# Kernel optimization log

Measured on AMD Instinct MI355X. Metric: run time of the kernel, lower is better.

The kernel has to match this reference:

```python
import jax, jax.numpy as jnp
import numpy as np

HEADS = 12
HEAD_SIZE = 64
NEG = 1e12


def setup_inputs() -> dict:
    key = jax.random.key(0)
    k1, k2 = jax.random.split(key)
    B, L, D = 32, 512, 768
    x = jax.random.normal(k1, (B, L, D), dtype=jnp.float32)
    mask = jnp.ones((B, L), dtype=jnp.float32)  # padding mask (1 = valid)
    W = jax.random.normal(k2, (D, HEADS * HEAD_SIZE * 2), dtype=jnp.float32) * 0.02
    b = jnp.zeros((HEADS * HEAD_SIZE * 2,), dtype=jnp.float32)
    return {"x": x, "mask": mask, "W": W, "b": b}


def _rope_sin_cos(L, s, dtype):
    # bert4keras SinusoidalPositionEmbedding: pe[..., ::2] = sin, pe[..., 1::2] = cos
    pos = jnp.arange(L, dtype=dtype)
    freq = jnp.power(10000.0, -2.0 * jnp.arange(s // 2, dtype=dtype) / s)
    ang = pos[:, None] * freq[None, :]            # [L, s/2]
    sin = jnp.repeat(jnp.sin(ang), 2, axis=-1)    # [L, s]
    cos = jnp.repeat(jnp.cos(ang), 2, axis=-1)    # [L, s]
    return sin, cos


def _rotate_half(t):
    # interleaved rotation: (-t1, t0, -t3, t2, ...)
    t2 = jnp.stack([-t[..., 1::2], t[..., ::2]], axis=-1)
    return t2.reshape(t.shape)


def reference(x, mask, W, b):
    B, L, D = x.shape
    s = HEAD_SIZE
    proj = x @ W + b                               # [B, L, heads*2s]
    proj = proj.reshape(B, L, HEADS, 2 * s)        # split-into-heads + stack
    qw, kw = proj[..., :s], proj[..., s:]
    sin, cos = _rope_sin_cos(L, s, x.dtype)
    sin = sin[None, :, None, :]                    # [1, L, 1, s]
    cos = cos[None, :, None, :]
    qw = qw * cos + _rotate_half(qw) * sin
    kw = kw * cos + _rotate_half(kw) * sin
    logits = jnp.einsum('bmhs,bnhs->bhmn', qw, kw)  # [B, H, L, L]
    m2 = mask[:, None, :, None]
    m3 = mask[:, None, None, :]
    logits = logits * m2 + (1.0 - m2) * -NEG
    logits = logits * m3 + (1.0 - m3) * -NEG
    tril = jnp.tril(jnp.ones((L, L), dtype=logits.dtype), -1)  # strictly lower
    logits = logits - tril * NEG                    # keep upper-triangular spans
    return (logits / jnp.sqrt(jnp.asarray(s, logits.dtype))).reshape(B, HEADS, L * L)
```

## Files before the change

kernel.cpp:

```cpp
#include <hip/hip_runtime.h>
#include <hip/hip_bf16.h>

#define HEADS 12
#define HSIZE 64
#define BATCH 32
#define SEQ 512
#define DIM 768
#define NOUT 1536
#define MROWS 16384
#define NEGV 1e12f

typedef __bf16 bf16x8 __attribute__((ext_vector_type(8)));
typedef float f32x4 __attribute__((ext_vector_type(4)));
typedef unsigned short u16x8 __attribute__((ext_vector_type(8)));
typedef unsigned short u16x4 __attribute__((ext_vector_type(4)));

__device__ __forceinline__ void async16(const void* g, void* l) {
  __builtin_amdgcn_global_load_lds(
      (const __attribute__((address_space(1))) void*)g,
      (__attribute__((address_space(3))) void*)l, 16, 0, 0);
}

__device__ __forceinline__ unsigned short f2b(float f) {
  union { __hip_bfloat16 h; unsigned short u; } cv;
  cv.h = __float2bfloat16(f);
  return cv.u;
}

__global__ void rope_table(float* __restrict__ sin_t, float* __restrict__ cos_t) {
  int idx = blockIdx.x * 256 + threadIdx.x;
  if (idx < SEQ * 32) {
    int pos = idx >> 5;
    int i = idx & 31;
    float freq = powf(10000.0f, -2.0f * (float)i / 64.0f);
    float ang = (float)pos * freq;
    sin_t[idx] = sinf(ang);
    cos_t[idx] = cosf(ang);
  }
}

__global__ void convert_x(const float* __restrict__ x, unsigned short* __restrict__ xb) {
  int idx = blockIdx.x * 256 + threadIdx.x;
  float4 v = ((const float4*)x)[idx];
  ushort4 o;
  o.x = f2b(v.x); o.y = f2b(v.y); o.z = f2b(v.z); o.w = f2b(v.w);
  ((ushort4*)xb)[idx] = o;
}

__global__ void transpose_w(const float* __restrict__ W, unsigned short* __restrict__ Wt) {
  __shared__ unsigned short tile[32][33];
  int n0 = blockIdx.x * 32;
  int k0 = blockIdx.y * 32;
  int tx = threadIdx.x & 31, ty = threadIdx.x >> 5;
#pragma unroll
  for (int j = 0; j < 32; j += 8) {
    tile[ty + j][tx] = f2b(W[(size_t)(k0 + ty + j) * NOUT + n0 + tx]);
  }
  __syncthreads();
#pragma unroll
  for (int j = 0; j < 32; j += 8) {
    Wt[(size_t)(n0 + ty + j) * DIM + k0 + tx] = tile[tx][ty + j];
  }
}

__global__ __launch_bounds__(256) void gemm_rope(
    const unsigned short* __restrict__ xb, const unsigned short* __restrict__ wt,
    const float* __restrict__ bias, const float* __restrict__ sin_t,
    const float* __restrict__ cos_t, unsigned short* __restrict__ q_ws,
    unsigned short* __restrict__ k_ws) {
  __shared__ __align__(16) unsigned short smem[128 * 136];
  unsigned short* As = smem;
  unsigned short* Bs = smem + 8192;
  const int tid = threadIdx.x;
  const int bx = blockIdx.x;
  const int tn = (bx % (NOUT / 128)) * 128;
  const int tm = (bx / (NOUT / 128)) * 128;
  const int wid = tid >> 6, lane = tid & 63;
  const int wm = (wid >> 1) * 64, wn = (wid & 1) * 64;
  const int lrow = lane & 15, lk = (lane >> 4) * 8;

  const int sr = tid >> 3;
  const int scb = (tid & 7) * 8;
  const unsigned short* a_src = xb + (size_t)(tm + sr) * DIM + scb;
  const unsigned short* b_src = wt + (size_t)(tn + sr) * DIM + scb;

  f32x4 acc[4][4] = {};
  for (int kt = 0; kt < 12; ++kt) {
    const int k0 = kt * 64;
#pragma unroll
    for (int p = 0; p < 4; ++p) {
      async16(a_src + (size_t)(p * 32) * DIM + k0, &As[(p * 32 + sr) * 64 + scb]);
      async16(b_src + (size_t)(p * 32) * DIM + k0, &Bs[(p * 32 + sr) * 64 + scb]);
    }
    __syncthreads();
#pragma unroll
    for (int ks = 0; ks < 2; ++ks) {
      bf16x8 nf[4], mf[4];
#pragma unroll
      for (int i = 0; i < 4; ++i) {
        nf[i] = *(const bf16x8*)&Bs[(wn + i * 16 + lrow) * 64 + ks * 32 + lk];
        mf[i] = *(const bf16x8*)&As[(wm + i * 16 + lrow) * 64 + ks * 32 + lk];
      }
#pragma unroll
      for (int ai = 0; ai < 4; ++ai)
#pragma unroll
        for (int bi = 0; bi < 4; ++bi)
          acc[ai][bi] = __builtin_amdgcn_mfma_f32_16x16x32_bf16(
              nf[ai], mf[bi], acc[ai][bi], 0, 0, 0);
    }
    __syncthreads();
  }

#pragma unroll
  for (int ai = 0; ai < 4; ++ai) {
    const int nloc = wn + ai * 16 + (lane >> 4) * 4;
    const int colb = tn + nloc;
    const int d0 = colb & 63;
    const float4 b4 = *(const float4*)&bias[colb];
#pragma unroll
    for (int bi = 0; bi < 4; ++bi) {
      const int mloc = wm + bi * 16 + lrow;
      const int pos = (tm + mloc) & (SEQ - 1);
      const float2 s01 = *(const float2*)&sin_t[pos * 32 + (d0 >> 1)];
      const float2 c01 = *(const float2*)&cos_t[pos * 32 + (d0 >> 1)];
      const float v0 = acc[ai][bi][0] + b4.x;
      const float v1 = acc[ai][bi][1] + b4.y;
      const float v2 = acc[ai][bi][2] + b4.z;
      const float v3 = acc[ai][bi][3] + b4.w;
      u16x4 pk;
      pk[0] = f2b(fmaf(v0, c01.x, -v1 * s01.x));
      pk[1] = f2b(fmaf(v1, c01.x,  v0 * s01.x));
      pk[2] = f2b(fmaf(v2, c01.y, -v3 * s01.y));
      pk[3] = f2b(fmaf(v3, c01.y,  v2 * s01.y));
      *(u16x4*)&smem[mloc * 136 + nloc] = pk;
    }
  }
  __syncthreads();

  const int bq = tm >> 9;
  const int pos0 = tm & (SEQ - 1);
  const int head = tn >> 7;
  const size_t rowbase = ((size_t)(bq * HEADS + head) * SEQ + pos0);
  const int rr = tid >> 3;
  const int cc = tid & 7;
#pragma unroll
  for (int p = 0; p < 4; ++p) {
    const int r = p * 32 + rr;
    u16x8 vq = *(const u16x8*)&smem[r * 136 + cc * 8];
    u16x8 vk = *(const u16x8*)&smem[r * 136 + 64 + cc * 8];
    *(u16x8*)&q_ws[(rowbase + r) * 64 + cc * 8] = vq;
    *(u16x8*)&k_ws[(rowbase + r) * 64 + cc * 8] = vk;
  }
}

__global__ __launch_bounds__(256) void qk_kernel(
    const unsigned short* __restrict__ q_ws, const unsigned short* __restrict__ k_ws,
    const float* __restrict__ mask, float* __restrict__ out) {
  __shared__ __align__(16) float ot[128 * 68];
  const int bx = blockIdx.x;
  const int bh = bx >> 2;
  const int tmm = (bx & 3) * 128;
  const int bidx = bh / HEADS;
  const int tid = threadIdx.x, wid = tid >> 6, lane = tid & 63;
  const int wm = wid * 32;
  const int lrow = lane & 15, lk = (lane >> 4) * 8;
  const unsigned short* Q = q_ws + ((size_t)bh << 15);
  const unsigned short* K = k_ws + ((size_t)bh << 15);

  bf16x8 qf[2][2];
#pragma unroll
  for (int mi = 0; mi < 2; ++mi)
#pragma unroll
    for (int ks = 0; ks < 2; ++ks)
      qf[mi][ks] = *(const bf16x8*)&Q[(size_t)(tmm + wm + mi * 16 + lrow) * 64 + ks * 32 + lk];

  float* obase = out + ((size_t)bh << 18);
  const float* mrow = mask + (size_t)bidx * SEQ;
  const int cc = tid & 15;
  const int rr = tid >> 4;

  for (int t = 0; t < 4; ++t) {
    const int tnn = t * 128;
    bf16x8 kf[8][2];
#pragma unroll
    for (int ni = 0; ni < 8; ++ni)
#pragma unroll
      for (int ks = 0; ks < 2; ++ks)
        kf[ni][ks] = *(const bf16x8*)&K[(size_t)(tnn + ni * 16 + lrow) * 64 + ks * 32 + lk];

    f32x4 acc[8][2] = {};
#pragma unroll
    for (int ks = 0; ks < 2; ++ks)
#pragma unroll
      for (int ni = 0; ni < 8; ++ni)
#pragma unroll
        for (int mi = 0; mi < 2; ++mi)
          acc[ni][mi] = __builtin_amdgcn_mfma_f32_16x16x32_bf16(
              kf[ni][ks], qf[mi][ks], acc[ni][mi], 0, 0, 0);

#pragma unroll
    for (int h = 0; h < 2; ++h) {
      __syncthreads();
#pragma unroll
      for (int ai = 0; ai < 4; ++ai) {
        const int nloc = ai * 16 + (lane >> 4) * 4;
#pragma unroll
        for (int mi = 0; mi < 2; ++mi) {
          const int mloc = wm + mi * 16 + lrow;
          *(f32x4*)&ot[mloc * 68 + nloc] = acc[h * 4 + ai][mi];
        }
      }
      __syncthreads();
      const int n0 = tnn + h * 64 + cc * 4;
      const f32x4 m3v = *(const f32x4*)&mrow[n0];
#pragma unroll
      for (int p = 0; p < 8; ++p) {
        const int r = p * 16 + rr;
        const int m = tmm + r;
        f32x4 v = *(const f32x4*)&ot[r * 68 + cc * 4];
        const float m2 = mrow[m];
        f32x4 o;
#pragma unroll
        for (int j = 0; j < 4; ++j) {
          float vv = v[j];
          vv = vv * m2 + (1.0f - m2) * (-NEGV);
          vv = vv * m3v[j] + (1.0f - m3v[j]) * (-NEGV);
          if (m > n0 + j) vv -= NEGV;
          o[j] = vv * 0.125f;
        }
        __builtin_nontemporal_store(o, (f32x4*)&obase[(size_t)m * 512 + n0]);
      }
    }
  }
}

extern "C" void kernel_launch(void* const* d_in, const int* in_sizes, int n_in,
                              void* d_out, int out_size, void* d_ws, size_t ws_size,
                              hipStream_t stream) {
  const float* x = (const float*)d_in[0];
  const float* mask = (const float*)d_in[1];
  const float* W = (const float*)d_in[2];
  const float* b = (const float*)d_in[3];
  float* out = (float*)d_out;

  char* ws = (char*)d_ws;
  float* sin_t = (float*)(ws + 0);
  float* cos_t = (float*)(ws + 65536);
  unsigned short* xb  = (unsigned short*)(ws + 131072);
  unsigned short* wt  = (unsigned short*)(ws + 25296896);
  unsigned short* q_ws = (unsigned short*)(ws + 27656192);
  unsigned short* k_ws = (unsigned short*)(ws + 52822016);

  rope_table<<<dim3(64), dim3(256), 0, stream>>>(sin_t, cos_t);
  convert_x<<<dim3(MROWS * DIM / 4 / 256), dim3(256), 0, stream>>>(x, xb);
  transpose_w<<<dim3(NOUT / 32, DIM / 32), dim3(256), 0, stream>>>(W, wt);
  gemm_rope<<<dim3((MROWS / 128) * (NOUT / 128)), dim3(256), 0, stream>>>(
      xb, wt, b, sin_t, cos_t, q_ws, k_ws);
  qk_kernel<<<dim3(BATCH * HEADS * 4), dim3(256), 0, stream>>>(q_ws, k_ws, mask, out);
}
```

Before: 519.3 us.

## Switch projection GEMM to FP8 MFMA with swizzled LDS layout

Converts x and W to FP8 (e4m3) instead of bf16 and runs the projection GEMM with the scaled 16x16x128 f8f6f4 MFMA, halving the K-loop trip count and the operand bytes loaded into LDS. It adds an XOR swizzle on LDS slots to avoid bank conflicts. FP8 sharply reduces input precision, so logits could drift beyond tolerance. The output qk kernel, which dominates the write traffic, is unchanged.

```diff
diff --git a/kernel.cpp b/kernel.cpp
--- a/kernel.cpp
+++ b/kernel.cpp
@@ -12,6 +12,8 @@
 
 typedef __bf16 bf16x8 __attribute__((ext_vector_type(8)));
 typedef float f32x4 __attribute__((ext_vector_type(4)));
+typedef int i32x4 __attribute__((ext_vector_type(4)));
+typedef int i32x8 __attribute__((ext_vector_type(8)));
 typedef unsigned short u16x8 __attribute__((ext_vector_type(8)));
 typedef unsigned short u16x4 __attribute__((ext_vector_type(4)));
 
@@ -25,6 +27,13 @@
   union { __hip_bfloat16 h; unsigned short u; } cv;
   cv.h = __float2bfloat16(f);
   return cv.u;
+}
+
+__device__ __forceinline__ unsigned int pk4_fp8(float a, float b, float c, float d) {
+  int v = 0;
+  v = __builtin_amdgcn_cvt_pk_fp8_f32(a, b, v, false);
+  v = __builtin_amdgcn_cvt_pk_fp8_f32(c, d, v, true);
+  return (unsigned int)v;
 }
 
 __global__ void rope_table(float* __restrict__ sin_t, float* __restrict__ cos_t) {
@@ -39,78 +48,98 @@
   }
 }
 
-__global__ void convert_x(const float* __restrict__ x, unsigned short* __restrict__ xb) {
+__global__ void convert_x(const float* __restrict__ x, unsigned int* __restrict__ xf8) {
   int idx = blockIdx.x * 256 + threadIdx.x;
-  float4 v = ((const float4*)x)[idx];
-  ushort4 o;
-  o.x = f2b(v.x); o.y = f2b(v.y); o.z = f2b(v.z); o.w = f2b(v.w);
-  ((ushort4*)xb)[idx] = o;
-}
-
-__global__ void transpose_w(const float* __restrict__ W, unsigned short* __restrict__ Wt) {
-  __shared__ unsigned short tile[32][33];
+  float4 v0 = ((const float4*)x)[idx * 2];
+  float4 v1 = ((const float4*)x)[idx * 2 + 1];
+  uint2 o;
+  o.x = pk4_fp8(v0.x, v0.y, v0.z, v0.w);
+  o.y = pk4_fp8(v1.x, v1.y, v1.z, v1.w);
+  ((uint2*)xf8)[idx] = o;
+}
+
+__global__ void transpose_w(const float* __restrict__ W, unsigned char* __restrict__ Wt) {
+  __shared__ float tile[32][33];
   int n0 = blockIdx.x * 32;
   int k0 = blockIdx.y * 32;
   int tx = threadIdx.x & 31, ty = threadIdx.x >> 5;
 #pragma unroll
   for (int j = 0; j < 32; j += 8) {
-    tile[ty + j][tx] = f2b(W[(size_t)(k0 + ty + j) * NOUT + n0 + tx]);
+    tile[ty + j][tx] = W[(size_t)(k0 + ty + j) * NOUT + n0 + tx];
   }
   __syncthreads();
 #pragma unroll
   for (int j = 0; j < 32; j += 8) {
-    Wt[(size_t)(n0 + ty + j) * DIM + k0 + tx] = tile[tx][ty + j];
+    const int n = n0 + ty + j;
+    Wt[(size_t)n * DIM + k0 + tx] =
+        (unsigned char)(pk4_fp8(tile[tx][ty + j], 0.f, 0.f, 0.f) & 0xFF);
   }
 }
 
 __global__ __launch_bounds__(256) void gemm_rope(
-    const unsigned short* __restrict__ xb, const unsigned short* __restrict__ wt,
+    const unsigned char* __restrict__ xf8, const unsigned char* __restrict__ wf8,
     const float* __restrict__ bias, const float* __restrict__ sin_t,
     const float* __restrict__ cos_t, unsigned short* __restrict__ q_ws,
     unsigned short* __restrict__ k_ws) {
-  __shared__ __align__(16) unsigned short smem[128 * 136];
-  unsigned short* As = smem;
-  unsigned short* Bs = smem + 8192;
+  __shared__ __align__(16) unsigned char smem[128 * 136 * 2];
+  unsigned char* As = smem;
+  unsigned char* Bs = smem + 16384;
   const int tid = threadIdx.x;
   const int bx = blockIdx.x;
   const int tn = (bx % (NOUT / 128)) * 128;
   const int tm = (bx / (NOUT / 128)) * 128;
   const int wid = tid >> 6, lane = tid & 63;
   const int wm = (wid >> 1) * 64, wn = (wid & 1) * 64;
-  const int lrow = lane & 15, lk = (lane >> 4) * 8;
-
-  const int sr = tid >> 3;
-  const int scb = (tid & 7) * 8;
-  const unsigned short* a_src = xb + (size_t)(tm + sr) * DIM + scb;
-  const unsigned short* b_src = wt + (size_t)(tn + sr) * DIM + scb;
+  const int lrow = lane & 15;
+  const int kc = lane >> 4;
+
+  const int srow = tid >> 3;
+  const int sslot = (tid & 7) ^ (srow & 7);
+  const unsigned char* a_src = xf8 + (size_t)(tm + srow) * DIM + sslot * 16;
+  const unsigned char* b_src = wf8 + (size_t)(tn + srow) * DIM + sslot * 16;
+  unsigned char* a_dst = As + tid * 16;
+  unsigned char* b_dst = Bs + tid * 16;
 
   f32x4 acc[4][4] = {};
-  for (int kt = 0; kt < 12; ++kt) {
-    const int k0 = kt * 64;
+  for (int kt = 0; kt < 6; ++kt) {
+    const int k0 = kt * 128;
 #pragma unroll
     for (int p = 0; p < 4; ++p) {
-      async16(a_src + (size_t)(p * 32) * DIM + k0, &As[(p * 32 + sr) * 64 + scb]);
-      async16(b_src + (size_t)(p * 32) * DIM + k0, &Bs[(p * 32 + sr) * 64 + scb]);
+      async16(a_src + (size_t)(p * 32) * DIM + k0, a_dst + p * 4096);
+      async16(b_src + (size_t)(p * 32) * DIM + k0, b_dst + p * 4096);
     }
     __syncthreads();
-#pragma unroll
-    for (int ks = 0; ks < 2; ++ks) {
-      bf16x8 nf[4], mf[4];
-#pragma unroll
-      for (int i = 0; i < 4; ++i) {
-        nf[i] = *(const bf16x8*)&Bs[(wn + i * 16 + lrow) * 64 + ks * 32 + lk];
-        mf[i] = *(const bf16x8*)&As[(wm + i * 16 + lrow) * 64 + ks * 32 + lk];
-      }
-#pragma unroll
-      for (int ai = 0; ai < 4; ++ai)
-#pragma unroll
-        for (int bi = 0; bi < 4; ++bi)
-          acc[ai][bi] = __builtin_amdgcn_mfma_f32_16x16x32_bf16(
-              nf[ai], mf[bi], acc[ai][bi], 0, 0, 0);
-    }
+    i32x8 nf[4], mf[4];
+#pragma unroll
+    for (int i = 0; i < 4; ++i) {
+      {
+        const int row = wn + i * 16 + lrow;
+        const int sw = lrow & 7;
+        union { i32x4 h[2]; i32x8 v; } u;
+        u.h[0] = *(const i32x4*)&Bs[row * 128 + ((kc * 2) ^ sw) * 16];
+        u.h[1] = *(const i32x4*)&Bs[row * 128 + ((kc * 2 + 1) ^ sw) * 16];
+        nf[i] = u.v;
+      }
+      {
+        const int row = wm + i * 16 + lrow;
+        const int sw = lrow & 7;
+        union { i32x4 h[2]; i32x8 v; } u;
+        u.h[0] = *(const i32x4*)&As[row * 128 + ((kc * 2) ^ sw) * 16];
+        u.h[1] = *(const i32x4*)&As[row * 128 + ((kc * 2 + 1) ^ sw) * 16];
+        mf[i] = u.v;
+      }
+    }
+#pragma unroll
+    for (int ai = 0; ai < 4; ++ai)
+#pragma unroll
+      for (int bi = 0; bi < 4; ++bi)
+        acc[ai][bi] = __builtin_amdgcn_mfma_scale_f32_16x16x128_f8f6f4(
+            nf[ai], mf[bi], acc[ai][bi], 0, 0,
+            0, 0x7F7F7F7F, 0, 0x7F7F7F7F);
     __syncthreads();
   }
 
+  unsigned short* osm = (unsigned short*)smem;
 #pragma unroll
   for (int ai = 0; ai < 4; ++ai) {
     const int nloc = wn + ai * 16 + (lane >> 4) * 4;
@@ -132,7 +161,7 @@
       pk[1] = f2b(fmaf(v1, c01.x,  v0 * s01.x));
       pk[2] = f2b(fmaf(v2, c01.y, -v3 * s01.y));
       pk[3] = f2b(fmaf(v3, c01.y,  v2 * s01.y));
-      *(u16x4*)&smem[mloc * 136 + nloc] = pk;
+      *(u16x4*)&osm[mloc * 136 + nloc] = pk;
     }
   }
   __syncthreads();
@@ -146,8 +175,8 @@
 #pragma unroll
   for (int p = 0; p < 4; ++p) {
     const int r = p * 32 + rr;
-    u16x8 vq = *(const u16x8*)&smem[r * 136 + cc * 8];
-    u16x8 vk = *(const u16x8*)&smem[r * 136 + 64 + cc * 8];
+    u16x8 vq = *(const u16x8*)&osm[r * 136 + cc * 8];
+    u16x8 vk = *(const u16x8*)&osm[r * 136 + 64 + cc * 8];
     *(u16x8*)&q_ws[(rowbase + r) * 64 + cc * 8] = vq;
     *(u16x8*)&k_ws[(rowbase + r) * 64 + cc * 8] = vk;
   }
@@ -246,15 +275,15 @@
   char* ws = (char*)d_ws;
   float* sin_t = (float*)(ws + 0);
   float* cos_t = (float*)(ws + 65536);
-  unsigned short* xb  = (unsigned short*)(ws + 131072);
-  unsigned short* wt  = (unsigned short*)(ws + 25296896);
-  unsigned short* q_ws = (unsigned short*)(ws + 27656192);
-  unsigned short* k_ws = (unsigned short*)(ws + 52822016);
+  unsigned char* xf8 = (unsigned char*)(ws + 131072);
+  unsigned char* wf8 = (unsigned char*)(ws + 12713984);
+  unsigned short* q_ws = (unsigned short*)(ws + 13893632);
+  unsigned short* k_ws = (unsigned short*)(ws + 39059456);
 
   rope_table<<<dim3(64), dim3(256), 0, stream>>>(sin_t, cos_t);
-  convert_x<<<dim3(MROWS * DIM / 4 / 256), dim3(256), 0, stream>>>(x, xb);
-  transpose_w<<<dim3(NOUT / 32, DIM / 32), dim3(256), 0, stream>>>(W, wt);
+  convert_x<<<dim3(MROWS * DIM / 8 / 256), dim3(256), 0, stream>>>(x, (unsigned int*)xf8);
+  transpose_w<<<dim3(NOUT / 32, DIM / 32), dim3(256), 0, stream>>>(W, wf8);
   gemm_rope<<<dim3((MROWS / 128) * (NOUT / 128)), dim3(256), 0, stream>>>(
-      xb, wt, b, sin_t, cos_t, q_ws, k_ws);
+      xf8, wf8, b, sin_t, cos_t, q_ws, k_ws);
   qk_kernel<<<dim3(BATCH * HEADS * 4), dim3(256), 0, stream>>>(q_ws, k_ws, mask, out);
 }
```

Result: faster. 499.4 us (-3.8%).
